# Kernel tuning notes

Measured on AMD Instinct MI355X. Metric: run time of the kernel, lower is better.

Reference implementation:

```python
import jax, jax.numpy as jnp
import numpy as np

N = 100000   # nodes
E = 1600000  # edges (avg degree 16)
IN, HID, CLS = 256, 128, 64

def setup_inputs() -> dict:
    key = jax.random.key(0)
    ks = jax.random.split(key, 7)
    x = jax.random.normal(ks[0], (N, IN), dtype=jnp.float32)
    src = jax.random.randint(ks[1], (E,), 0, N, dtype=jnp.int32)
    dst = jax.random.randint(ks[2], (E,), 0, N, dtype=jnp.int32)
    # glorot-ish init for GraphConv weights
    W1 = jax.random.normal(ks[3], (IN, HID), dtype=jnp.float32) * (1.0 / np.sqrt(IN))
    W2 = jax.random.normal(ks[4], (HID, HID), dtype=jnp.float32) * (1.0 / np.sqrt(HID))
    W3 = jax.random.normal(ks[5], (HID, CLS), dtype=jnp.float32) * (1.0 / np.sqrt(HID))
    b1 = jnp.zeros((HID,), jnp.float32)
    b2 = jnp.zeros((HID,), jnp.float32)
    b3 = jnp.zeros((CLS,), jnp.float32)
    return {"x": x, "src": src, "dst": dst, "W1": W1, "b1": b1,
            "W2": W2, "b2": b2, "W3": W3, "b3": b3}


def _graph_conv(h, src, dst, W, b, out_norm, in_norm):
    """DGL GraphConv with norm='both', allow_zero_in_degree=True."""
    in_f, out_f = W.shape
    h = h * out_norm[:, None]                 # src-side degree norm
    if in_f > out_f:
        # transform first (fewer flops), then aggregate
        h = h @ W
        agg = jax.ops.segment_sum(h[src], dst, num_segments=N)
    else:
        agg = jax.ops.segment_sum(h[src], dst, num_segments=N)
        agg = agg @ W
    return agg * in_norm[:, None] + b         # dst-side norm + bias


def reference(x, src, dst, W1, b1, W2, b2, W3, b3):
    ones = jnp.ones((E,), jnp.float32)
    out_deg = jax.ops.segment_sum(ones, src, num_segments=N)
    in_deg = jax.ops.segment_sum(ones, dst, num_segments=N)
    out_norm = jnp.clip(out_deg, 1.0) ** -0.5
    in_norm = jnp.clip(in_deg, 1.0) ** -0.5

    h = _graph_conv(x, src, dst, W1, b1, out_norm, in_norm)
    h = jax.nn.relu(h)  # dropout = identity in eval mode
    h = _graph_conv(h, src, dst, W2, b2, out_norm, in_norm)
    h = jax.nn.relu(h)
    h = _graph_conv(h, src, dst, W3, b3, out_norm, in_norm)
    return h
```

## Files before the change

### kernel.cpp

```cpp
#include <hip/hip_runtime.h>

#define NN 100000
#define NE 1600000
#define FIN 256
#define FHID 128
#define FCLS 64

#define SH1 9
#define P1 196
#define EPB_H 2048
#define NBH ((NE + EPB_H - 1) / EPB_H)
#define EPB_P 4096
#define NBP ((NE + EPB_P - 1) / EPB_P)
#define BROWS 4

typedef _Float16 f16;
typedef __attribute__((ext_vector_type(8))) _Float16 f16x8;
typedef __attribute__((ext_vector_type(2))) _Float16 f16x2;
typedef __attribute__((ext_vector_type(4))) float f32x4;
typedef __attribute__((ext_vector_type(2))) float f32x2;

__global__ __launch_bounds__(256) void k_histA(const int* __restrict__ src, const int* __restrict__ dst,
                                               int* __restrict__ outdeg, int* __restrict__ hist2d) {
  __shared__ int lh[P1];
  int t = threadIdx.x;
  for (int i = t; i < P1; i += 256) lh[i] = 0;
  __syncthreads();
  int base = blockIdx.x * EPB_H;
  int cnt = NE - base; if (cnt > EPB_H) cnt = EPB_H;
  for (int i = t; i < cnt; i += 256) {
    atomicAdd(&outdeg[src[base + i]], 1);
    atomicAdd(&lh[dst[base + i] >> SH1], 1);
  }
  __syncthreads();
  for (int i = t; i < P1; i += 256) hist2d[blockIdx.x * P1 + i] = lh[i];
}

__global__ __launch_bounds__(256) void k_colscan(const int* __restrict__ hist2d, int* __restrict__ colpre,
                                                 int* __restrict__ totals) {
  __shared__ int sm[256];
  int p = blockIdx.x;
  int t = threadIdx.x;
  int vals[BROWS];
  int lsum = 0;
  int b0 = t * BROWS;
#pragma unroll
  for (int i = 0; i < BROWS; ++i) {
    int b = b0 + i;
    int v = (b < NBH) ? hist2d[b * P1 + p] : 0;
    vals[i] = v;
    lsum += v;
  }
  int x = lsum;
  sm[t] = x;
  __syncthreads();
  for (int off = 1; off < 256; off <<= 1) {
    int y = (t >= off) ? sm[t - off] : 0;
    __syncthreads();
    x += y;
    sm[t] = x;
    __syncthreads();
  }
  int run = x - lsum;
#pragma unroll
  for (int i = 0; i < BROWS; ++i) {
    int b = b0 + i;
    if (b < NBH) colpre[b * P1 + p] = run;
    run += vals[i];
  }
  if (t == 255) totals[p] = x;
}

__global__ __launch_bounds__(256) void k_pbase(const int* __restrict__ totals, int* __restrict__ pbase,
                                               int* __restrict__ rp) {
  __shared__ int sm[256];
  int t = threadIdx.x;
  int v = (t < P1) ? totals[t] : 0;
  int x = v;
  sm[t] = x;
  __syncthreads();
  for (int off = 1; off < 256; off <<= 1) {
    int y = (t >= off) ? sm[t - off] : 0;
    __syncthreads();
    x += y;
    sm[t] = x;
    __syncthreads();
  }
  if (t < P1) pbase[t] = x - v;
  if (t == 0) rp[NN] = NE;
}

__global__ __launch_bounds__(256) void k_place(const int* __restrict__ src, const int* __restrict__ dst,
                                               const int* __restrict__ hist2d, const int* __restrict__ colpre,
                                               const int* __restrict__ pbase, unsigned* __restrict__ staged) {
  __shared__ unsigned buf[EPB_P];
  __shared__ unsigned char prt[EPB_P];
  __shared__ int lofs[P1], lcur[P1], lbase[P1];
  __shared__ int sm[256];
  int t = threadIdx.x;
  int b = blockIdx.x;
  int v = 0;
  if (t < P1) {
    int f0 = 2 * b, f1 = 2 * b + 1;
    v = hist2d[f0 * P1 + t];
    if (f1 < NBH) v += hist2d[f1 * P1 + t];
    lbase[t] = pbase[t] + colpre[f0 * P1 + t];
    lcur[t] = 0;
  }
  int x = v;
  sm[t] = x;
  __syncthreads();
  for (int off = 1; off < 256; off <<= 1) {
    int y = (t >= off) ? sm[t - off] : 0;
    __syncthreads();
    x += y;
    sm[t] = x;
    __syncthreads();
  }
  if (t < P1) lofs[t] = x - v;
  __syncthreads();
  int base = b * EPB_P;
  int cnt = NE - base; if (cnt > EPB_P) cnt = EPB_P;
  for (int i = t; i < cnt; i += 256) {
    int s = src[base + i], d = dst[base + i];
    int p = d >> SH1;
    int pos = lofs[p] + atomicAdd(&lcur[p], 1);
    buf[pos] = ((unsigned)s << SH1) | (unsigned)(d & 511);
    prt[pos] = (unsigned char)p;
  }
  __syncthreads();
  for (int i = t; i < cnt; i += 256) {
    int p = prt[i];
    staged[lbase[p] + (i - lofs[p])] = buf[i];
  }
}

__global__ __launch_bounds__(512) void k_buildp(const unsigned* __restrict__ staged, const int* __restrict__ totals,
                                                const int* __restrict__ pbase, const int* __restrict__ outdeg,
                                                int* __restrict__ rp, float* __restrict__ inorm,
                                                float* __restrict__ onorm, int* __restrict__ csr) {
  __shared__ int lcnt[512], lofs[512], lcur[512];
  int p = blockIdx.x, t = threadIdx.x;
  int pb = pbase[p], cnt = totals[p];
  lcnt[t] = 0;
  __syncthreads();
  const unsigned* sp = staged + pb;
  for (int i = t; i < cnt; i += 512) atomicAdd(&lcnt[sp[i] & 511], 1);
  __syncthreads();
  int v = lcnt[t];
  int x = v;
  lofs[t] = x;
  __syncthreads();
  for (int off = 1; off < 512; off <<= 1) {
    int y = (t >= off) ? lofs[t - off] : 0;
    __syncthreads();
    x += y;
    lofs[t] = x;
    __syncthreads();
  }
  int excl = x - v;
  lofs[t] = excl;
  lcur[t] = 0;
  int node = (p << SH1) + t;
  if (node < NN) {
    rp[node] = pb + excl;
    int dg = v < 1 ? 1 : v;
    inorm[node] = rsqrtf((float)dg);
    int od = outdeg[node];
    if (od < 1) od = 1;
    onorm[node] = rsqrtf((float)od);
  }
  __syncthreads();
  for (int i = t; i < cnt; i += 512) {
    unsigned e = sp[i];
    int d = e & 511;
    int pos = pb + lofs[d] + atomicAdd(&lcur[d], 1);
    csr[pos] = (int)(e >> SH1);
  }
}

template <int K, int NW>
__global__ __launch_bounds__(256) void k_packw(const float* __restrict__ W, f16* __restrict__ Wp) {
  int idx = blockIdx.x * 256 + threadIdx.x;
  if (idx >= K * NW) return;
  constexpr int nT = NW / 16;
  int i = idx & 7;
  int l = (idx >> 3) & 63;
  int rest = idx >> 9;
  int t = rest % nT;
  int s = rest / nT;
  int k = s * 32 + (l >> 4) * 8 + i;
  int n = t * 16 + (l & 15);
  Wp[idx] = (f16)W[k * NW + n];
}

template <int K, int NW, int MODE>
__global__ __launch_bounds__(256) void k_gemm(const void* __restrict__ Asrc, const f16* __restrict__ Wp,
                                              const float* __restrict__ onorm, const float* __restrict__ bias,
                                              f16* __restrict__ Out) {
  constexpr int nS = K / 32, nT = NW / 16;
  int lane = threadIdx.x & 63;
  int w = threadIdx.x >> 6;
  int bm = blockIdx.x * 64 + w * 16;
  int arow = bm + (lane & 15);
  int koff = (lane >> 4) * 8;
  bool rowok = arow < NN;

  f32x4 acc[nT];
#pragma unroll
  for (int t = 0; t < nT; ++t) acc[t] = (f32x4){0.f, 0.f, 0.f, 0.f};

  float ascale = 0.0f;
  if (MODE == 0) ascale = rowok ? onorm[arow] : 0.0f;

  for (int s = 0; s < nS; ++s) {
    f16x8 a = {};
    if (rowok) {
      if (MODE == 0) {
        const float* ap = (const float*)Asrc + (size_t)arow * K + s * 32 + koff;
        f32x4 v0 = *(const f32x4*)ap;
        f32x4 v1 = *(const f32x4*)(ap + 4);
#pragma unroll
        for (int j = 0; j < 4; ++j) {
          a[j] = (f16)(v0[j] * ascale);
          a[4 + j] = (f16)(v1[j] * ascale);
        }
      } else {
        a = *(const f16x8*)((const f16*)Asrc + ((size_t)s * NN + arow) * 32 + koff);
      }
    }
    const f16* bp = Wp + ((size_t)(s * nT) * 64 + lane) * 8;
#pragma unroll
    for (int t = 0; t < nT; ++t) {
      f16x8 bfr = *(const f16x8*)(bp + t * 512);
      acc[t] = __builtin_amdgcn_mfma_f32_16x16x32_f16(a, bfr, acc[t], 0, 0, 0);
    }
  }

  int crow0 = bm + (lane >> 4) * 4;
  int ccol = lane & 15;
#pragma unroll
  for (int t = 0; t < nT; ++t) {
#pragma unroll
    for (int r = 0; r < 4; ++r) {
      int row = crow0 + r;
      if (row >= NN) continue;
      int col = t * 16 + ccol;
      float v = acc[t][r];
      if (MODE == 2) v = fmaxf(v + bias[col], 0.f) * onorm[row];
      Out[((size_t)(col >> 5) * NN + row) * 32 + (col & 31)] = (f16)v;
    }
  }
}

#define LCSR_CAP 1408
template <int NS, int MODE>
__global__ __launch_bounds__(256) void k_aggs(const f16* __restrict__ src_arr, const int* __restrict__ rp,
                                              const int* __restrict__ csr, const float* __restrict__ inorm,
                                              const float* __restrict__ onorm, const float* __restrict__ bias,
                                              void* __restrict__ outp) {
  constexpr int XPS = 8 / NS;
  constexpr int BPS = (NN + 63) / 64;
  __shared__ int lcsr[LCSR_CAP];
  int bid = blockIdx.x;
  int r = bid & 7;
  int slice = r / XPS;
  int w = (bid >> 3) * XPS + (r % XPS);
  if (w >= BPS) return;
  int t = threadIdx.x;
  int nbase = w * 64;
  int nlim = nbase + 64; if (nlim > NN) nlim = NN;
  int first = rp[nbase];
  int last = rp[nlim];
  int span = last - first;
  bool useLds = (span <= LCSR_CAP);
  if (useLds) {
    for (int i = t; i < span; i += 256) lcsr[i] = csr[first + i];
  }
  __syncthreads();
  int node = nbase + (t >> 2);
  if (node >= NN) return;
  int q = t & 3;
  int beg = rp[node], end = rp[node + 1];
  const char* sbp = (const char*)src_arr + ((size_t)slice * NN * 32 + q * 8) * 2;

  float acc[8];
#pragma unroll
  for (int j = 0; j < 8; ++j) acc[j] = 0.f;

  if (useLds) {
    int le = beg - first, lend = end - first;
    for (; le + 7 < lend; le += 8) {
      int x0 = lcsr[le], x1 = lcsr[le + 1], x2 = lcsr[le + 2], x3 = lcsr[le + 3];
      int x4 = lcsr[le + 4], x5 = lcsr[le + 5], x6 = lcsr[le + 6], x7 = lcsr[le + 7];
      f16x8 v0 = *(const f16x8*)(sbp + ((size_t)(unsigned)x0 << 6));
      f16x8 v1 = *(const f16x8*)(sbp + ((size_t)(unsigned)x1 << 6));
      f16x8 v2 = *(const f16x8*)(sbp + ((size_t)(unsigned)x2 << 6));
      f16x8 v3 = *(const f16x8*)(sbp + ((size_t)(unsigned)x3 << 6));
      f16x8 v4 = *(const f16x8*)(sbp + ((size_t)(unsigned)x4 << 6));
      f16x8 v5 = *(const f16x8*)(sbp + ((size_t)(unsigned)x5 << 6));
      f16x8 v6 = *(const f16x8*)(sbp + ((size_t)(unsigned)x6 << 6));
      f16x8 v7 = *(const f16x8*)(sbp + ((size_t)(unsigned)x7 << 6));
#pragma unroll
      for (int j = 0; j < 8; ++j) {
        float s01 = (float)v0[j] + (float)v1[j];
        float s23 = (float)v2[j] + (float)v3[j];
        float s45 = (float)v4[j] + (float)v5[j];
        float s67 = (float)v6[j] + (float)v7[j];
        acc[j] += (s01 + s23) + (s45 + s67);
      }
    }
    for (; le + 3 < lend; le += 4) {
      int x0 = lcsr[le], x1 = lcsr[le + 1], x2 = lcsr[le + 2], x3 = lcsr[le + 3];
      f16x8 v0 = *(const f16x8*)(sbp + ((size_t)(unsigned)x0 << 6));
      f16x8 v1 = *(const f16x8*)(sbp + ((size_t)(unsigned)x1 << 6));
      f16x8 v2 = *(const f16x8*)(sbp + ((size_t)(unsigned)x2 << 6));
      f16x8 v3 = *(const f16x8*)(sbp + ((size_t)(unsigned)x3 << 6));
#pragma unroll
      for (int j = 0; j < 8; ++j)
        acc[j] += ((float)v0[j] + (float)v1[j]) + ((float)v2[j] + (float)v3[j]);
    }
    for (; le < lend; ++le) {
      f16x8 v0 = *(const f16x8*)(sbp + ((size_t)(unsigned)lcsr[le] << 6));
#pragma unroll
      for (int j = 0; j < 8; ++j) acc[j] += (float)v0[j];
    }
  } else {
    for (int e = beg; e < end; ++e) {
      f16x8 v0 = *(const f16x8*)(sbp + ((size_t)(unsigned)csr[e] << 6));
#pragma unroll
      for (int j = 0; j < 8; ++j) acc[j] += (float)v0[j];
    }
  }

  float inn = inorm[node];
  int gfb = slice * 32 + q * 8;
  if (MODE == 0) {
    float on = onorm[node];
    f16x8 o;
#pragma unroll
    for (int j = 0; j < 8; ++j) o[j] = (f16)(fmaxf(acc[j] * inn + bias[gfb + j], 0.f) * on);
    *(f16x8*)((f16*)outp + ((size_t)slice * NN + node) * 32 + q * 8) = o;
  } else if (MODE == 1) {
    f16x8 o;
#pragma unroll
    for (int j = 0; j < 8; ++j) o[j] = (f16)(acc[j] * inn);
    *(f16x8*)((f16*)outp + ((size_t)slice * NN + node) * 32 + q * 8) = o;
  } else {
    float* op = (float*)outp + (size_t)node * (NS * 32) + gfb;
    f32x4 o0, o1;
#pragma unroll
    for (int j = 0; j < 4; ++j) {
      o0[j] = acc[j] * inn + bias[gfb + j];
      o1[j] = acc[4 + j] * inn + bias[gfb + 4 + j];
    }
    *(f32x4*)op = o0;
    *(f32x4*)(op + 4) = o1;
  }
}

extern "C" void kernel_launch(void* const* d_in, const int* in_sizes, int n_in,
                              void* d_out, int out_size, void* d_ws, size_t ws_size,
                              hipStream_t stream) {
  const float* x = (const float*)d_in[0];
  const int* src = (const int*)d_in[1];
  const int* dst = (const int*)d_in[2];
  const float* W1 = (const float*)d_in[3];
  const float* b1 = (const float*)d_in[4];
  const float* W2 = (const float*)d_in[5];
  const float* b2 = (const float*)d_in[6];
  const float* W3 = (const float*)d_in[7];
  const float* b3 = (const float*)d_in[8];

  char* base = (char*)d_ws;
  size_t off = 0;
  auto take = [&](size_t bytes) -> void* {
    void* r = base + off;
    off += (bytes + 255) & ~(size_t)255;
    return r;
  };
  int* outdeg = (int*)take((size_t)NN * 4);
  float* onorm = (float*)take((size_t)NN * 4);
  float* inorm = (float*)take((size_t)NN * 4);
  int* rp = (int*)take((size_t)(NN + 1) * 4);
  int* totals = (int*)take((size_t)P1 * 4);
  int* pbase = (int*)take((size_t)P1 * 4);
  int* hist2d = (int*)take((size_t)NBH * P1 * 4);
  int* colpre = (int*)take((size_t)NBH * P1 * 4);
  unsigned* staged = (unsigned*)take((size_t)NE * 4);
  int* csr = (int*)take((size_t)NE * 4);
  f16* W1p = (f16*)take((size_t)FIN * FHID * 2);
  f16* W2p = (f16*)take((size_t)FHID * FHID * 2);
  f16* W3p = (f16*)take((size_t)FHID * FCLS * 2);
  f16* B1 = (f16*)take((size_t)NN * FHID * 2);
  f16* B2 = (f16*)take((size_t)NN * FHID * 2);

  hipMemsetAsync(outdeg, 0, (size_t)NN * 4, stream);

  k_histA<<<NBH, 256, 0, stream>>>(src, dst, outdeg, hist2d);
  k_colscan<<<P1, 256, 0, stream>>>(hist2d, colpre, totals);
  k_pbase<<<1, 256, 0, stream>>>(totals, pbase, rp);
  k_place<<<NBP, 256, 0, stream>>>(src, dst, hist2d, colpre, pbase, staged);
  k_buildp<<<P1, 512, 0, stream>>>(staged, totals, pbase, outdeg, rp, inorm, onorm, csr);

  k_packw<FIN, FHID><<<(FIN * FHID + 255) / 256, 256, 0, stream>>>(W1, W1p);
  k_packw<FHID, FHID><<<(FHID * FHID + 255) / 256, 256, 0, stream>>>(W2, W2p);
  k_packw<FHID, FCLS><<<(FHID * FCLS + 255) / 256, 256, 0, stream>>>(W3, W3p);

  const int gemm_grid = (NN + 63) / 64;
  const int bps = (NN + 63) / 64;
  const int agg4_grid = ((bps + 1) / 2) * 8;
  const int agg2_grid = ((bps + 3) / 4) * 8;
  k_gemm<FIN, FHID, 0><<<gemm_grid, 256, 0, stream>>>(x, W1p, onorm, nullptr, B1);
  k_aggs<4, 0><<<agg4_grid, 256, 0, stream>>>(B1, rp, csr, inorm, onorm, b1, B2);
  k_aggs<4, 1><<<agg4_grid, 256, 0, stream>>>(B2, rp, csr, inorm, nullptr, nullptr, B1);
  k_gemm<FHID, FHID, 2><<<gemm_grid, 256, 0, stream>>>(B1, W2p, onorm, b2, B2);
  k_gemm<FHID, FCLS, 1><<<gemm_grid, 256, 0, stream>>>(B2, W3p, nullptr, nullptr, B1);
  k_aggs<2, 2><<<agg2_grid, 256, 0, stream>>>(B1, rp, csr, inorm, nullptr, b3, d_out);
}
```

Measured before the change: 342.9 us.

## Compute out-degree via partitioned bucket sort instead of global atomics

Replaces the per-edge global atomicAdd on outdeg, plus its memset, with a second partitioned histogram and placement pass keyed on src. Source ids are scattered as 16-bit local ids into a staging buffer, and a new per-partition kernel counts them in shared memory to produce onorm. This aims to remove contended random global atomics, at the cost of extra LDS use in k_place, more scan work, an extra kernel, and about 3.2MB of extra traffic.

```diff
diff --git a/kernel.cpp b/kernel.cpp
--- a/kernel.cpp
+++ b/kernel.cpp
@@ -21,25 +21,34 @@
 typedef __attribute__((ext_vector_type(2))) float f32x2;
 
 __global__ __launch_bounds__(256) void k_histA(const int* __restrict__ src, const int* __restrict__ dst,
-                                               int* __restrict__ outdeg, int* __restrict__ hist2d) {
-  __shared__ int lh[P1];
+                                               int* __restrict__ hist2d, int* __restrict__ shist2d) {
+  __shared__ int lh[P1], lhS[P1];
   int t = threadIdx.x;
-  for (int i = t; i < P1; i += 256) lh[i] = 0;
+  for (int i = t; i < P1; i += 256) { lh[i] = 0; lhS[i] = 0; }
   __syncthreads();
   int base = blockIdx.x * EPB_H;
   int cnt = NE - base; if (cnt > EPB_H) cnt = EPB_H;
   for (int i = t; i < cnt; i += 256) {
-    atomicAdd(&outdeg[src[base + i]], 1);
     atomicAdd(&lh[dst[base + i] >> SH1], 1);
-  }
-  __syncthreads();
-  for (int i = t; i < P1; i += 256) hist2d[blockIdx.x * P1 + i] = lh[i];
-}
-
-__global__ __launch_bounds__(256) void k_colscan(const int* __restrict__ hist2d, int* __restrict__ colpre,
-                                                 int* __restrict__ totals) {
+    atomicAdd(&lhS[src[base + i] >> SH1], 1);
+  }
+  __syncthreads();
+  for (int i = t; i < P1; i += 256) {
+    hist2d[blockIdx.x * P1 + i] = lh[i];
+    shist2d[blockIdx.x * P1 + i] = lhS[i];
+  }
+}
+
+__global__ __launch_bounds__(256) void k_colscan2(const int* __restrict__ hist2d, const int* __restrict__ shist2d,
+                                                  int* __restrict__ colpre, int* __restrict__ colpreS,
+                                                  int* __restrict__ totals, int* __restrict__ totalsS) {
   __shared__ int sm[256];
-  int p = blockIdx.x;
+  int bp = blockIdx.x;
+  bool isS = bp >= P1;
+  int p = isS ? bp - P1 : bp;
+  const int* h = isS ? shist2d : hist2d;
+  int* cp = isS ? colpreS : colpre;
+  int* tt = isS ? totalsS : totals;
   int t = threadIdx.x;
   int vals[BROWS];
   int lsum = 0;
@@ -47,7 +56,7 @@
 #pragma unroll
   for (int i = 0; i < BROWS; ++i) {
     int b = b0 + i;
-    int v = (b < NBH) ? hist2d[b * P1 + p] : 0;
+    int v = (b < NBH) ? h[b * P1 + p] : 0;
     vals[i] = v;
     lsum += v;
   }
@@ -65,14 +74,15 @@
 #pragma unroll
   for (int i = 0; i < BROWS; ++i) {
     int b = b0 + i;
-    if (b < NBH) colpre[b * P1 + p] = run;
+    if (b < NBH) cp[b * P1 + p] = run;
     run += vals[i];
   }
-  if (t == 255) totals[p] = x;
-}
-
-__global__ __launch_bounds__(256) void k_pbase(const int* __restrict__ totals, int* __restrict__ pbase,
-                                               int* __restrict__ rp) {
+  if (t == 255) tt[p] = x;
+}
+
+__global__ __launch_bounds__(256) void k_pbase2(const int* __restrict__ totals, const int* __restrict__ totalsS,
+                                                int* __restrict__ pbase, int* __restrict__ pbaseS,
+                                                int* __restrict__ rp) {
   __shared__ int sm[256];
   int t = threadIdx.x;
   int v = (t < P1) ? totals[t] : 0;
@@ -87,25 +97,45 @@
     __syncthreads();
   }
   if (t < P1) pbase[t] = x - v;
+  __syncthreads();
+  int vS = (t < P1) ? totalsS[t] : 0;
+  int xS = vS;
+  sm[t] = xS;
+  __syncthreads();
+  for (int off = 1; off < 256; off <<= 1) {
+    int y = (t >= off) ? sm[t - off] : 0;
+    __syncthreads();
+    xS += y;
+    sm[t] = xS;
+    __syncthreads();
+  }
+  if (t < P1) pbaseS[t] = xS - vS;
   if (t == 0) rp[NN] = NE;
 }
 
 __global__ __launch_bounds__(256) void k_place(const int* __restrict__ src, const int* __restrict__ dst,
-                                               const int* __restrict__ hist2d, const int* __restrict__ colpre,
-                                               const int* __restrict__ pbase, unsigned* __restrict__ staged) {
+                                               const int* __restrict__ hist2d, const int* __restrict__ shist2d,
+                                               const int* __restrict__ colpre, const int* __restrict__ colpreS,
+                                               const int* __restrict__ pbase, const int* __restrict__ pbaseS,
+                                               unsigned* __restrict__ staged, unsigned short* __restrict__ stagedS) {
   __shared__ unsigned buf[EPB_P];
+  __shared__ unsigned bufS[EPB_P];
   __shared__ unsigned char prt[EPB_P];
   __shared__ int lofs[P1], lcur[P1], lbase[P1];
+  __shared__ int lofsS[P1], lcurS[P1], lbaseS[P1];
   __shared__ int sm[256];
   int t = threadIdx.x;
   int b = blockIdx.x;
-  int v = 0;
+  int f0 = 2 * b, f1 = 2 * b + 1;
+  int v = 0, vS = 0;
   if (t < P1) {
-    int f0 = 2 * b, f1 = 2 * b + 1;
     v = hist2d[f0 * P1 + t];
-    if (f1 < NBH) v += hist2d[f1 * P1 + t];
+    vS = shist2d[f0 * P1 + t];
+    if (f1 < NBH) { v += hist2d[f1 * P1 + t]; vS += shist2d[f1 * P1 + t]; }
     lbase[t] = pbase[t] + colpre[f0 * P1 + t];
+    lbaseS[t] = pbaseS[t] + colpreS[f0 * P1 + t];
     lcur[t] = 0;
+    lcurS[t] = 0;
   }
   int x = v;
   sm[t] = x;
@@ -119,6 +149,19 @@
   }
   if (t < P1) lofs[t] = x - v;
   __syncthreads();
+  int xS = vS;
+  sm[t] = xS;
+  __syncthreads();
+  for (int off = 1; off < 256; off <<= 1) {
+    int y = (t >= off) ? sm[t - off] : 0;
+    __syncthreads();
+    xS += y;
+    sm[t] = xS;
+    __syncthreads();
+  }
+  if (t < P1) lofsS[t] = xS - vS;
+  __syncthreads();
+
   int base = b * EPB_P;
   int cnt = NE - base; if (cnt > EPB_P) cnt = EPB_P;
   for (int i = t; i < cnt; i += 256) {
@@ -127,18 +170,23 @@
     int pos = lofs[p] + atomicAdd(&lcur[p], 1);
     buf[pos] = ((unsigned)s << SH1) | (unsigned)(d & 511);
     prt[pos] = (unsigned char)p;
+    int pS = s >> SH1;
+    int posS = lofsS[pS] + atomicAdd(&lcurS[pS], 1);
+    bufS[posS] = (unsigned)s;
   }
   __syncthreads();
   for (int i = t; i < cnt; i += 256) {
     int p = prt[i];
     staged[lbase[p] + (i - lofs[p])] = buf[i];
+    unsigned sv = bufS[i];
+    int pS = sv >> SH1;
+    stagedS[lbaseS[pS] + (i - lofsS[pS])] = (unsigned short)(sv & 511);
   }
 }
 
 __global__ __launch_bounds__(512) void k_buildp(const unsigned* __restrict__ staged, const int* __restrict__ totals,
-                                                const int* __restrict__ pbase, const int* __restrict__ outdeg,
-                                                int* __restrict__ rp, float* __restrict__ inorm,
-                                                float* __restrict__ onorm, int* __restrict__ csr) {
+                                                const int* __restrict__ pbase, int* __restrict__ rp,
+                                                float* __restrict__ inorm, int* __restrict__ csr) {
   __shared__ int lcnt[512], lofs[512], lcur[512];
   int p = blockIdx.x, t = threadIdx.x;
   int pb = pbase[p], cnt = totals[p];
@@ -166,9 +214,6 @@
     rp[node] = pb + excl;
     int dg = v < 1 ? 1 : v;
     inorm[node] = rsqrtf((float)dg);
-    int od = outdeg[node];
-    if (od < 1) od = 1;
-    onorm[node] = rsqrtf((float)od);
   }
   __syncthreads();
   for (int i = t; i < cnt; i += 512) {
@@ -176,6 +221,25 @@
     int d = e & 511;
     int pos = pb + lofs[d] + atomicAdd(&lcur[d], 1);
     csr[pos] = (int)(e >> SH1);
+  }
+}
+
+__global__ __launch_bounds__(512) void k_countS(const unsigned short* __restrict__ stagedS,
+                                                const int* __restrict__ totalsS, const int* __restrict__ pbaseS,
+                                                float* __restrict__ onorm) {
+  __shared__ int lcnt[512];
+  int p = blockIdx.x, t = threadIdx.x;
+  int pb = pbaseS[p], cnt = totalsS[p];
+  lcnt[t] = 0;
+  __syncthreads();
+  const unsigned short* sp = stagedS + pb;
+  for (int i = t; i < cnt; i += 512) atomicAdd(&lcnt[sp[i]], 1);
+  __syncthreads();
+  int node = (p << SH1) + t;
+  if (node < NN) {
+    int od = lcnt[t];
+    if (od < 1) od = 1;
+    onorm[node] = rsqrtf((float)od);
   }
 }
 
@@ -379,15 +443,19 @@
     off += (bytes + 255) & ~(size_t)255;
     return r;
   };
-  int* outdeg = (int*)take((size_t)NN * 4);
   float* onorm = (float*)take((size_t)NN * 4);
   float* inorm = (float*)take((size_t)NN * 4);
   int* rp = (int*)take((size_t)(NN + 1) * 4);
   int* totals = (int*)take((size_t)P1 * 4);
+  int* totalsS = (int*)take((size_t)P1 * 4);
   int* pbase = (int*)take((size_t)P1 * 4);
+  int* pbaseS = (int*)take((size_t)P1 * 4);
   int* hist2d = (int*)take((size_t)NBH * P1 * 4);
+  int* shist2d = (int*)take((size_t)NBH * P1 * 4);
   int* colpre = (int*)take((size_t)NBH * P1 * 4);
+  int* colpreS = (int*)take((size_t)NBH * P1 * 4);
   unsigned* staged = (unsigned*)take((size_t)NE * 4);
+  unsigned short* stagedS = (unsigned short*)take((size_t)NE * 2);
   int* csr = (int*)take((size_t)NE * 4);
   f16* W1p = (f16*)take((size_t)FIN * FHID * 2);
   f16* W2p = (f16*)take((size_t)FHID * FHID * 2);
@@ -395,13 +463,12 @@
   f16* B1 = (f16*)take((size_t)NN * FHID * 2);
   f16* B2 = (f16*)take((size_t)NN * FHID * 2);
 
-  hipMemsetAsync(outdeg, 0, (size_t)NN * 4, stream);
-
-  k_histA<<<NBH, 256, 0, stream>>>(src, dst, outdeg, hist2d);
-  k_colscan<<<P1, 256, 0, stream>>>(hist2d, colpre, totals);
-  k_pbase<<<1, 256, 0, stream>>>(totals, pbase, rp);
-  k_place<<<NBP, 256, 0, stream>>>(src, dst, hist2d, colpre, pbase, staged);
-  k_buildp<<<P1, 512, 0, stream>>>(staged, totals, pbase, outdeg, rp, inorm, onorm, csr);
+  k_histA<<<NBH, 256, 0, stream>>>(src, dst, hist2d, shist2d);
+  k_colscan2<<<2 * P1, 256, 0, stream>>>(hist2d, shist2d, colpre, colpreS, totals, totalsS);
+  k_pbase2<<<1, 256, 0, stream>>>(totals, totalsS, pbase, pbaseS, rp);
+  k_place<<<NBP, 256, 0, stream>>>(src, dst, hist2d, shist2d, colpre, colpreS, pbase, pbaseS, staged, stagedS);
+  k_buildp<<<P1, 512, 0, stream>>>(staged, totals, pbase, rp, inorm, csr);
+  k_countS<<<P1, 512, 0, stream>>>(stagedS, totalsS, pbaseS, onorm);
 
   k_packw<FIN, FHID><<<(FIN * FHID + 255) / 256, 256, 0, stream>>>(W1, W1p);
   k_packw<FHID, FHID><<<(FHID * FHID + 255) / 256, 256, 0, stream>>>(W2, W2p);
```

Result: faster. 286.2 us (-16.5%).
